# Performance work log

Measured on AMD Instinct MI355X. Metric: run time of the kernel, lower is better.

Reference implementation:

```python
import jax, jax.numpy as jnp
import numpy as np

VOCAB = 65
N_EMBD = 32
HEAD = 16
BLOCK = 8
B = 65536


def setup_inputs() -> dict:
    key = jax.random.key(0)
    ks = jax.random.split(key, 12)
    idx = jax.random.randint(ks[0], (B, BLOCK), 0, VOCAB)
    targets = jax.random.randint(ks[1], (B, BLOCK), 0, VOCAB)
    s = 0.02
    tok_emb = jax.random.normal(ks[2], (VOCAB, N_EMBD), jnp.float32) * s
    pos_emb = jax.random.normal(ks[3], (BLOCK, N_EMBD), jnp.float32) * s
    Wk = jax.random.normal(ks[4], (N_EMBD, HEAD), jnp.float32) * s
    bk = jnp.zeros((HEAD,), jnp.float32)
    Wq = jax.random.normal(ks[5], (N_EMBD, HEAD), jnp.float32) * s
    bq = jnp.zeros((HEAD,), jnp.float32)
    Wv = jax.random.normal(ks[6], (N_EMBD, HEAD), jnp.float32) * s
    bv = jnp.zeros((HEAD,), jnp.float32)
    Wlm = jax.random.normal(ks[7], (HEAD, VOCAB), jnp.float32) * s
    blm = jnp.zeros((VOCAB,), jnp.float32)
    return {"idx": idx, "targets": targets, "tok_emb": tok_emb, "pos_emb": pos_emb,
            "Wk": Wk, "bk": bk, "Wq": Wq, "bq": bq, "Wv": Wv, "bv": bv,
            "Wlm": Wlm, "blm": blm}


def reference(idx, targets, tok_emb, pos_emb, Wk, bk, Wq, bq, Wv, bv, Wlm, blm):
    Bsz, T = idx.shape
    x = tok_emb[idx] + pos_emb[None, :T, :]                  # (B,T,C)
    k = x @ Wk + bk                                          # (B,T,H)
    q = x @ Wq + bq
    wei = jnp.einsum('bth,bsh->bts', q, k) * (HEAD ** -0.5)  # (B,T,T)
    tril = jnp.tril(jnp.ones((T, T), bool))
    wei = jnp.where(tril[None], wei, -jnp.inf)
    # NOTE: original torch code uses F.softmax(wei, dim=1) — over the QUERY axis.
    wei = jax.nn.softmax(wei, axis=1)
    v = x @ Wv + bv
    attn = jnp.einsum('bts,bsh->bth', wei, v)                # (B,T,H)
    logits = attn @ Wlm + blm                                # (B,T,V)
    logits_flat = logits.reshape(Bsz * T, VOCAB)
    tgt_flat = targets.reshape(Bsz * T)
    logp = jax.nn.log_softmax(logits_flat, axis=-1)
    loss = -jnp.mean(jnp.take_along_axis(logp, tgt_flat[:, None], axis=-1))
    return logits_flat, loss
```

## Files before the change

kernel.cpp:

```cpp
#include <hip/hip_runtime.h>
#include <hip/hip_bf16.h>

#define NVOC 65
#define NE   32
#define HD   16
#define NB   65536
#define NROWS (NB * 8)
#define NLOG  (NROWS * NVOC)


static __device__ __forceinline__ float readlane_f(float v, int l) {
  return __uint_as_float(__builtin_amdgcn_readlane(__float_as_uint(v), l));
}

__global__ __launch_bounds__(1024) void bigram_tables(
    const float* __restrict__ tok, const float* __restrict__ pos,
    const float* __restrict__ Wk, const float* __restrict__ bk,
    const float* __restrict__ Wq, const float* __restrict__ bq,
    const float* __restrict__ Wv, const float* __restrict__ bv,
    const float* __restrict__ Wlm, float* __restrict__ ws)
{
  __shared__ float S[8416];
  const int tid = threadIdx.x;
  if (tid == 0) ws[0] = 0.f;
  for (int o = tid; o < 2080; o += 1024) S[o] = tok[o];
  for (int o = tid; o < 256;  o += 1024) S[2080 + o] = pos[o];
  for (int o = tid; o < 512;  o += 1024) {
    S[2336 + o] = Wq[o]; S[2848 + o] = Wk[o]; S[3360 + o] = Wv[o];
  }
  for (int o = tid; o < 1040; o += 1024) S[3872 + o] = Wlm[o];
  __syncthreads();

  for (int o = tid; o < 1168; o += 1024) {
    if (o < 1040) {
      const int a = o >> 4, h = o & 15;
      float sq = 0.f, sk = 0.f, sv = 0.f;
      #pragma unroll
      for (int c = 0; c < NE; ++c) {
        const float e = S[a*32 + c];
        sq = fmaf(e, S[2336 + c*16 + h], sq);
        sk = fmaf(e, S[2848 + c*16 + h], sk);
        sv = fmaf(e, S[3360 + c*16 + h], sv);
      }
      S[4912 + o] = sq; S[5952 + o] = sk; S[6992 + o] = sv;
    } else {
      const int o2 = o - 1040, t = o2 >> 4, h = o2 & 15;
      float sq = bq[h], sk = bk[h], sv = bv[h];
      #pragma unroll
      for (int c = 0; c < NE; ++c) {
        const float e = S[2080 + t*32 + c];
        sq = fmaf(e, S[2336 + c*16 + h], sq);
        sk = fmaf(e, S[2848 + c*16 + h], sk);
        sv = fmaf(e, S[3360 + c*16 + h], sv);
      }
      S[8032 + o2] = sq; S[8160 + o2] = sk; S[8288 + o2] = sv;
    }
  }
  __syncthreads();

  float* wsTab = ws + 16;
  for (int o = tid; o < 10074; o += 1024) {
    float r = 0.f; int dst;
    if (o < 4225) {
      const int a = o / 65, b = o % 65;
      #pragma unroll
      for (int h = 0; h < HD; ++h) r = fmaf(S[4912 + a*16 + h], S[5952 + b*16 + h], r);
      r *= 0.25f; dst = o;
    } else if (o < 4745) {
      const int o2 = o - 4225, a = o2 >> 3, s2 = o2 & 7;
      #pragma unroll
      for (int h = 0; h < HD; ++h) r = fmaf(S[4912 + a*16 + h], S[8160 + s2*16 + h], r);
      r *= 0.25f; dst = 8450 + o2;
    } else if (o < 5265) {
      const int o2 = o - 4745, t2 = o2 / 65, b = o2 % 65;
      #pragma unroll
      for (int h = 0; h < HD; ++h) r = fmaf(S[8032 + t2*16 + h], S[5952 + b*16 + h], r);
      r *= 0.25f; dst = 8970 + o2;
    } else if (o < 5329) {
      const int o2 = o - 5265, t2 = o2 >> 3, s2 = o2 & 7;
      #pragma unroll
      for (int h = 0; h < HD; ++h) r = fmaf(S[8032 + t2*16 + h], S[8160 + s2*16 + h], r);
      r *= 0.25f; dst = 9490 + o2;
    } else if (o < 9554) {
      const int o2 = o - 5329, a = o2 / 65, j = o2 % 65;
      #pragma unroll
      for (int h = 0; h < HD; ++h) r = fmaf(S[6992 + a*16 + h], S[3872 + h*65 + j], r);
      dst = 4225 + o2;
    } else {
      const int o2 = o - 9554, s2 = o2 / 65, j = o2 % 65;
      #pragma unroll
      for (int h = 0; h < HD; ++h) r = fmaf(S[8288 + s2*16 + h], S[3872 + h*65 + j], r);
      dst = o;
    }
    wsTab[dst] = r;
  }
}

__global__ __launch_bounds__(512, 6) void bigram_main(
    const int* __restrict__ idx, const int* __restrict__ tgt,
    const float* __restrict__ blm, const float* __restrict__ ws,
    float* __restrict__ wsacc, float* __restrict__ out)
{
  __shared__ __align__(16) float S[10074];
  __shared__ float red[8];
  const int tid = threadIdx.x;
  const float* wsTab = ws + 16;
  {
    const float4* t4 = (const float4*)wsTab;
    float4* s4 = (float4*)S;
    for (int o = tid; o < 2518; o += 512) s4[o] = t4[o];
    if (tid < 2) S[10072 + tid] = wsTab[10072 + tid];
  }
  const int lane = tid & 63;
  const int w    = tid >> 6;
  const int t    = lane >> 3;
  const int s    = lane & 7;
  const float blmj  = blm[lane];
  const float blm64 = blm[64];
  const int gw = blockIdx.x * 8 + w;
  const int iv = idx[gw*64 + lane];
  const int tv = tgt[gw*64 + lane];
  __syncthreads();

  const float g4 = S[9490 + lane];
  float pvl[8], pvl64[8];
  #pragma unroll
  for (int k = 0; k < 8; ++k) {
    pvl[k]   = S[9554 + k*65 + lane];
    pvl64[k] = S[9554 + k*65 + 64];
  }

  float acc_lsm = 0.f, acc_tl = 0.f;
  for (int itb = 0; itb < 8; ++itb) {
    const int base = itb * 8;
    const int av  = __shfl(iv, base + s);
    const int a_t = __shfl(iv, base + t);
    float wr = S[a_t*65 + av] + S[8450 + a_t*8 + s] + S[8970 + t*65 + av] + g4;
    float e = (t >= s) ? __expf(wr) : 0.f;
    float sm = e;
    sm += __shfl_xor(sm, 8); sm += __shfl_xor(sm, 16); sm += __shfl_xor(sm, 32);
    const float wsm = __fdividef(e, sm);
    float Ms[8], Ms64[8];
    #pragma unroll
    for (int k = 0; k < 8; ++k) {
      const int ak = __builtin_amdgcn_readlane(iv, base + k);
      Ms[k]   = S[4225 + ak*65 + lane] + pvl[k];
      Ms64[k] = S[4225 + ak*65 + 64]  + pvl64[k];
    }
    const int rowbase = (gw*8 + itb) * 520;
    float ee[8];
    #pragma unroll
    for (int tt = 0; tt < 8; ++tt) {
      float lg = blmj, lg64 = blm64;
      #pragma unroll
      for (int k = 0; k < 8; ++k) {
        const float wk = readlane_f(wsm, tt*8 + k);
        lg   = fmaf(wk, Ms[k],   lg);
        lg64 = fmaf(wk, Ms64[k], lg64);
      }
      out[rowbase + tt*65 + lane] = lg;
      if (lane == 63) out[rowbase + tt*65 + 64] = lg64;
      float x = __expf(lg);
      if (lane == 63) x += __expf(lg64);
      ee[tt] = x;
      const int tg  = __builtin_amdgcn_readlane(tv, base + tt);
      const int tgc = tg < 64 ? tg : 0;
      const float l_at_tg = readlane_f(lg, tgc);
      acc_tl += (tg < 64) ? l_at_tg : lg64;
    }
    #pragma unroll
    for (int tt = 0; tt < 8; ++tt) {
      ee[tt] += __shfl_xor(ee[tt], 1);
      ee[tt] += __shfl_xor(ee[tt], 2);
      ee[tt] += __shfl_xor(ee[tt], 4);
    }
    const int u = lane & 7;
    float r01 = (u & 1) ? ee[1] : ee[0];
    float r23 = (u & 1) ? ee[3] : ee[2];
    float r45 = (u & 1) ? ee[5] : ee[4];
    float r67 = (u & 1) ? ee[7] : ee[6];
    float r03 = (u & 2) ? r23 : r01;
    float r47 = (u & 2) ? r67 : r45;
    float r   = (u & 4) ? r47 : r03;
    r += __shfl_xor(r, 8); r += __shfl_xor(r, 16); r += __shfl_xor(r, 32);
    acc_lsm += __logf(r);
  }
  float v = acc_lsm * 0.125f - acc_tl * 0.015625f;
  v += __shfl_xor(v, 1); v += __shfl_xor(v, 2);  v += __shfl_xor(v, 4);
  v += __shfl_xor(v, 8); v += __shfl_xor(v, 16); v += __shfl_xor(v, 32);
  if (lane == 0) red[w] = v;
  __syncthreads();
  if (tid == 0) {
    float acc = red[0] + red[1] + red[2] + red[3] + red[4] + red[5] + red[6] + red[7];
    atomicAdd(wsacc, acc);
  }
}

__global__ void bigram_fin(const float* __restrict__ ws, float* __restrict__ out) {
  if (threadIdx.x == 0) out[NLOG] = ws[0] * (1.0f / (float)NROWS);
}

extern "C" void kernel_launch(void* const* d_in, const int* in_sizes, int n_in,
                              void* d_out, int out_size, void* d_ws, size_t ws_size,
                              hipStream_t stream) {
  const int* idx = (const int*)d_in[0];
  const int* tgt = (const int*)d_in[1];
  float* ws = (float*)d_ws;
  float* out = (float*)d_out;

  bigram_tables<<<1, 1024, 0, stream>>>((const float*)d_in[2], (const float*)d_in[3],
                                        (const float*)d_in[4], (const float*)d_in[5],
                                        (const float*)d_in[6], (const float*)d_in[7],
                                        (const float*)d_in[8], (const float*)d_in[9],
                                        (const float*)d_in[10], ws);
  bigram_main<<<1024, 512, 0, stream>>>(idx, tgt, (const float*)d_in[11], ws, ws, out);
  bigram_fin<<<1, 1, 0, stream>>>(ws, out);
}
```

Baseline: 209.5 us.

## Spread table precompute across blocks and compute vocab column 64 with lane-parallel reduction

The table kernel now runs on 40 blocks of 256 threads instead of one block of 1024. Each block redundantly builds the shared projections and then computes a single table entry per thread, which shortens the serial prologue. In the main kernel, logit column 64 was computed redundantly in every lane and then stored and exponentiated only by lane 63. It is now computed once per (t, s) lane with a shuffle reduction and merged into the softmax denominator. Logit stores use nontemporal hints. The trade-off is redundant projection work in every table block and extra shuffles in the main loop.

New measurement: 234.9 us. 1.12x slower.

```diff
diff --git a/kernel.cpp b/kernel.cpp
--- a/kernel.cpp
+++ b/kernel.cpp
@@ -13,7 +13,7 @@
   return __uint_as_float(__builtin_amdgcn_readlane(__float_as_uint(v), l));
 }
 
-__global__ __launch_bounds__(1024) void bigram_tables(
+__global__ __launch_bounds__(256) void bigram_tables(
     const float* __restrict__ tok, const float* __restrict__ pos,
     const float* __restrict__ Wk, const float* __restrict__ bk,
     const float* __restrict__ Wq, const float* __restrict__ bq,
@@ -22,16 +22,16 @@
 {
   __shared__ float S[8416];
   const int tid = threadIdx.x;
-  if (tid == 0) ws[0] = 0.f;
-  for (int o = tid; o < 2080; o += 1024) S[o] = tok[o];
-  for (int o = tid; o < 256;  o += 1024) S[2080 + o] = pos[o];
-  for (int o = tid; o < 512;  o += 1024) {
+  if (blockIdx.x == 0 && tid == 0) ws[0] = 0.f;
+  for (int o = tid; o < 2080; o += 256) S[o] = tok[o];
+  S[2080 + tid] = pos[tid];
+  for (int o = tid; o < 512;  o += 256) {
     S[2336 + o] = Wq[o]; S[2848 + o] = Wk[o]; S[3360 + o] = Wv[o];
   }
-  for (int o = tid; o < 1040; o += 1024) S[3872 + o] = Wlm[o];
-  __syncthreads();
-
-  for (int o = tid; o < 1168; o += 1024) {
+  for (int o = tid; o < 1040; o += 256) S[3872 + o] = Wlm[o];
+  __syncthreads();
+
+  for (int o = tid; o < 1168; o += 256) {
     if (o < 1040) {
       const int a = o >> 4, h = o & 15;
       float sq = 0.f, sk = 0.f, sv = 0.f;
@@ -58,42 +58,42 @@
   }
   __syncthreads();
 
+  const int o = blockIdx.x * 256 + tid;
+  if (o >= 10074) return;
   float* wsTab = ws + 16;
-  for (int o = tid; o < 10074; o += 1024) {
-    float r = 0.f; int dst;
-    if (o < 4225) {
-      const int a = o / 65, b = o % 65;
-      #pragma unroll
-      for (int h = 0; h < HD; ++h) r = fmaf(S[4912 + a*16 + h], S[5952 + b*16 + h], r);
-      r *= 0.25f; dst = o;
-    } else if (o < 4745) {
-      const int o2 = o - 4225, a = o2 >> 3, s2 = o2 & 7;
-      #pragma unroll
-      for (int h = 0; h < HD; ++h) r = fmaf(S[4912 + a*16 + h], S[8160 + s2*16 + h], r);
-      r *= 0.25f; dst = 8450 + o2;
-    } else if (o < 5265) {
-      const int o2 = o - 4745, t2 = o2 / 65, b = o2 % 65;
-      #pragma unroll
-      for (int h = 0; h < HD; ++h) r = fmaf(S[8032 + t2*16 + h], S[5952 + b*16 + h], r);
-      r *= 0.25f; dst = 8970 + o2;
-    } else if (o < 5329) {
-      const int o2 = o - 5265, t2 = o2 >> 3, s2 = o2 & 7;
-      #pragma unroll
-      for (int h = 0; h < HD; ++h) r = fmaf(S[8032 + t2*16 + h], S[8160 + s2*16 + h], r);
-      r *= 0.25f; dst = 9490 + o2;
-    } else if (o < 9554) {
-      const int o2 = o - 5329, a = o2 / 65, j = o2 % 65;
-      #pragma unroll
-      for (int h = 0; h < HD; ++h) r = fmaf(S[6992 + a*16 + h], S[3872 + h*65 + j], r);
-      dst = 4225 + o2;
-    } else {
-      const int o2 = o - 9554, s2 = o2 / 65, j = o2 % 65;
-      #pragma unroll
-      for (int h = 0; h < HD; ++h) r = fmaf(S[8288 + s2*16 + h], S[3872 + h*65 + j], r);
-      dst = o;
-    }
-    wsTab[dst] = r;
-  }
+  float r = 0.f; int dst;
+  if (o < 4225) {
+    const int a = o / 65, b = o % 65;
+    #pragma unroll
+    for (int h = 0; h < HD; ++h) r = fmaf(S[4912 + a*16 + h], S[5952 + b*16 + h], r);
+    r *= 0.25f; dst = o;
+  } else if (o < 4745) {
+    const int o2 = o - 4225, a = o2 >> 3, s2 = o2 & 7;
+    #pragma unroll
+    for (int h = 0; h < HD; ++h) r = fmaf(S[4912 + a*16 + h], S[8160 + s2*16 + h], r);
+    r *= 0.25f; dst = 8450 + o2;
+  } else if (o < 5265) {
+    const int o2 = o - 4745, t2 = o2 / 65, b = o2 % 65;
+    #pragma unroll
+    for (int h = 0; h < HD; ++h) r = fmaf(S[8032 + t2*16 + h], S[5952 + b*16 + h], r);
+    r *= 0.25f; dst = 8970 + o2;
+  } else if (o < 5329) {
+    const int o2 = o - 5265, t2 = o2 >> 3, s2 = o2 & 7;
+    #pragma unroll
+    for (int h = 0; h < HD; ++h) r = fmaf(S[8032 + t2*16 + h], S[8160 + s2*16 + h], r);
+    r *= 0.25f; dst = 9490 + o2;
+  } else if (o < 9554) {
+    const int o2 = o - 5329, a = o2 / 65, j = o2 % 65;
+    #pragma unroll
+    for (int h = 0; h < HD; ++h) r = fmaf(S[6992 + a*16 + h], S[3872 + h*65 + j], r);
+    dst = 4225 + o2;
+  } else {
+    const int o2 = o - 9554, s2 = o2 / 65, j = o2 % 65;
+    #pragma unroll
+    for (int h = 0; h < HD; ++h) r = fmaf(S[8288 + s2*16 + h], S[3872 + h*65 + j], r);
+    dst = o;
+  }
+  wsTab[dst] = r;
 }
 
 __global__ __launch_bounds__(512, 6) void bigram_main(
@@ -123,12 +123,10 @@
   __syncthreads();
 
   const float g4 = S[9490 + lane];
-  float pvl[8], pvl64[8];
+  float pvl[8];
   #pragma unroll
-  for (int k = 0; k < 8; ++k) {
-    pvl[k]   = S[9554 + k*65 + lane];
-    pvl64[k] = S[9554 + k*65 + 64];
-  }
+  for (int k = 0; k < 8; ++k) pvl[k] = S[9554 + k*65 + lane];
+  const float pvl64s = S[9554 + s*65 + 64];
 
   float acc_lsm = 0.f, acc_tl = 0.f;
   for (int itb = 0; itb < 8; ++itb) {
@@ -140,34 +138,34 @@
     float sm = e;
     sm += __shfl_xor(sm, 8); sm += __shfl_xor(sm, 16); sm += __shfl_xor(sm, 32);
     const float wsm = __fdividef(e, sm);
-    float Ms[8], Ms64[8];
+    const float M64s = S[4225 + av*65 + 64] + pvl64s;
+    float y = wsm * M64s;
+    y += __shfl_xor(y, 1); y += __shfl_xor(y, 2); y += __shfl_xor(y, 4);
+    const float lg64t = blm64 + y;
+    float Ms[8];
     #pragma unroll
     for (int k = 0; k < 8; ++k) {
       const int ak = __builtin_amdgcn_readlane(iv, base + k);
-      Ms[k]   = S[4225 + ak*65 + lane] + pvl[k];
-      Ms64[k] = S[4225 + ak*65 + 64]  + pvl64[k];
+      Ms[k] = S[4225 + ak*65 + lane] + pvl[k];
     }
     const int rowbase = (gw*8 + itb) * 520;
     float ee[8];
     #pragma unroll
     for (int tt = 0; tt < 8; ++tt) {
-      float lg = blmj, lg64 = blm64;
+      float lg = blmj;
       #pragma unroll
-      for (int k = 0; k < 8; ++k) {
-        const float wk = readlane_f(wsm, tt*8 + k);
-        lg   = fmaf(wk, Ms[k],   lg);
-        lg64 = fmaf(wk, Ms64[k], lg64);
-      }
-      out[rowbase + tt*65 + lane] = lg;
-      if (lane == 63) out[rowbase + tt*65 + 64] = lg64;
-      float x = __expf(lg);
-      if (lane == 63) x += __expf(lg64);
-      ee[tt] = x;
+      for (int k = 0; k < 8; ++k)
+        lg = fmaf(readlane_f(wsm, tt*8 + k), Ms[k], lg);
+      __builtin_nontemporal_store(lg, out + rowbase + tt*65 + lane);
+      ee[tt] = __expf(lg);
       const int tg  = __builtin_amdgcn_readlane(tv, base + tt);
       const int tgc = tg < 64 ? tg : 0;
       const float l_at_tg = readlane_f(lg, tgc);
-      acc_tl += (tg < 64) ? l_at_tg : lg64;
-    }
+      acc_tl += (tg < 64) ? l_at_tg : readlane_f(lg64t, tt*8);
+    }
+    if (s == 0)
+      __builtin_nontemporal_store(lg64t, out + rowbase + t*65 + 64);
+    const float x64 = __expf(lg64t);
     #pragma unroll
     for (int tt = 0; tt < 8; ++tt) {
       ee[tt] += __shfl_xor(ee[tt], 1);
@@ -183,6 +181,7 @@
     float r47 = (u & 2) ? r67 : r45;
     float r   = (u & 4) ? r47 : r03;
     r += __shfl_xor(r, 8); r += __shfl_xor(r, 16); r += __shfl_xor(r, 32);
+    r += __shfl(x64, u * 8);
     acc_lsm += __logf(r);
   }
   float v = acc_lsm * 0.125f - acc_tl * 0.015625f;
@@ -208,7 +207,7 @@
   float* ws = (float*)d_ws;
   float* out = (float*)d_out;
 
-  bigram_tables<<<1, 1024, 0, stream>>>((const float*)d_in[2], (const float*)d_in[3],
+  bigram_tables<<<40, 256, 0, stream>>>((const float*)d_in[2], (const float*)d_in[3],
                                         (const float*)d_in[4], (const float*)d_in[5],
                                         (const float*)d_in[6], (const float*)d_in[7],
                                         (const float*)d_in[8], (const float*)d_in[9],
```
